# Optimization experiments

Measured on AMD Instinct MI355X. Metric: run time of the kernel, lower is better.

Reference implementation:

```python
import jax, jax.numpy as jnp
import numpy as np

GRID = 48          # static voxel-grid extent (positions generated in [0, GRID)^3)
K = 3              # kernel size per axis (odd -> offset = 0.0 in the original module)
C = (K - 1) // 2   # kernel center
VOXEL_SIZE = 1.0   # forward default in DeConvolution.call


def setup_inputs() -> dict:
    key = jax.random.key(0)
    k1, k2 = jax.random.split(key)
    g = np.arange(GRID)
    coords = np.stack(np.meshgrid(g, g, g, indexing='ij'), axis=-1).reshape(-1, 3)
    # sparse input point cloud: half-density sub-lattice; dense-ish output lattice
    inp_positions = jnp.asarray(coords[coords.sum(axis=1) % 2 == 0], jnp.float32)  # (55296, 3)
    out_positions = jnp.asarray(coords, jnp.float32)                               # (110592, 3)
    n_in = inp_positions.shape[0]
    cin, cout = 256, 256
    features = jax.random.normal(k1, (n_in, cin), dtype=jnp.float32)
    # SparseConvTranspose kernel: [k, k, k, in_channels, filters]
    W = jax.random.normal(k2, (K, K, K, cin, cout), dtype=jnp.float32) * 0.05
    return {"features": features, "inp_positions": inp_positions,
            "out_positions": out_positions, "W": W}


def reference(features, inp_positions, out_positions, W):
    # Voxelize. kernel is odd -> offset = 0.0, so v = floor(p / voxel_size).
    vin = jnp.floor(inp_positions / VOXEL_SIZE).astype(jnp.int32)   # (N_in, 3)
    vout = jnp.floor(out_positions / VOXEL_SIZE).astype(jnp.int32)  # (N_out, 3)
    n_in = features.shape[0]

    # Dense voxel -> input-row hash grid (-1 = empty voxel).
    grid = jnp.full((GRID, GRID, GRID), -1, dtype=jnp.int32)
    grid = grid.at[vin[:, 0], vin[:, 1], vin[:, 2]].set(
        jnp.arange(n_in, dtype=jnp.int32))

    out = jnp.zeros((vout.shape[0], W.shape[-1]), dtype=features.dtype)
    # Transposed sparse conv: out[j] += W[v_in - v_out + C] @ feat[i]
    # Static 27-tap loop; each tap is a gather + dense GEMM.
    for dx in range(-C, C + 1):
        for dy in range(-C, C + 1):
            for dz in range(-C, C + 1):
                u = vout + jnp.array([dx, dy, dz], dtype=jnp.int32)   # source voxel
                inb = jnp.all((u >= 0) & (u < GRID), axis=1)
                uc = jnp.clip(u, 0, GRID - 1)
                idx = grid[uc[:, 0], uc[:, 1], uc[:, 2]]              # (N_out,)
                valid = inb & (idx >= 0)
                g = jnp.where(valid[:, None],
                              features[jnp.maximum(idx, 0)], 0.0)     # (N_out, Cin)
                out = out + g @ W[dx + C, dy + C, dz + C]             # (N_out, Cout)
    return out
```

## Files before the change

kernel.cpp:

```cpp
#include <hip/hip_runtime.h>

#define NIN   55296
#define CIN   256
#define COUT  256
#define NTH   512
#define NBLK  432

typedef __attribute__((ext_vector_type(8))) _Float16 half8;
typedef __attribute__((ext_vector_type(4))) _Float16 half4;
typedef __attribute__((ext_vector_type(4))) float f32x4;

typedef const __attribute__((address_space(1))) void* gp_t;
typedef __attribute__((address_space(3))) void* lp_t;
__device__ __forceinline__ void gload16(const void* g, char* l) {
  __builtin_amdgcn_global_load_lds((gp_t)g, (lp_t)l, 16, 0, 0);
}

__global__ void k_feat_cvt(const float* __restrict__ f, _Float16* __restrict__ o, int n4) {
  int i = blockIdx.x * blockDim.x + threadIdx.x;
  if (i >= n4) return;
  f32x4 v = ((const f32x4*)f)[i];
  half4 r;
  r[0] = (_Float16)v[0]; r[1] = (_Float16)v[1];
  r[2] = (_Float16)v[2]; r[3] = (_Float16)v[3];
  ((half4*)o)[i] = r;
}

__global__ void k_w_cvt(const float* __restrict__ W, _Float16* __restrict__ Wt,
                        float* __restrict__ zeros) {
  int i = blockIdx.x * blockDim.x + threadIdx.x;
  int d   = i >> 16;
  int rem = i & 65535;
  int n   = rem >> 8;
  int k   = rem & 255;
  Wt[i] = (_Float16)W[(d << 16) + (k << 8) + n];
  if (blockIdx.x == 0 && threadIdx.x < 128) zeros[threadIdx.x] = 0.0f;
}

__global__ __launch_bounds__(NTH, 2)
void k_conv8(const _Float16* __restrict__ featb, const _Float16* __restrict__ wt,
             const char* __restrict__ zeros, float* __restrict__ out) {
  extern __shared__ char lds[];
  int* orow = (int*)(lds + 131072);

  const int braw = blockIdx.x;
  const int b    = (braw & 7) * 54 + (braw >> 3);
  const int p    = b & 1;
  const int tile = b >> 1;

  const int tid = threadIdx.x;
  const int w   = tid >> 6;
  const int l   = tid & 63;

  const int rr  = w * 16 + (l >> 2);
  const int swz = ((l & 3) ^ ((l >> 3) & 3)) * 16;

  int xs[2], ys[2], zs[2];
#pragma unroll
  for (int q = 0; q < 2; ++q) {
    int e = tile * 256 + q * 128 + rr;
    int c = e / 24;
    int zi = e - c * 24;
    int x = c / 48;
    int y = c - x * 48;
    xs[q] = x; ys[q] = y; zs[q] = 2 * zi + ((x + y + p) & 1);
  }
  const char* wtc   = (const char*)wt;
  const char* featc = (const char*)featb;
  const int bro0 = rr * 512 + swz;
  const int bro1 = (128 + rr) * 512 + swz;

  const int wm = w >> 2, wn = w & 3;
  const int lr = l & 15, kg = l >> 4;
  const int rsw = (kg ^ ((lr >> 1) & 3)) * 16;
  const int aRd = (wm * 128 + lr) * 64 + rsw;
  const int bRd = (wn * 64 + lr) * 64 + rsw;

  if (tid < 256) {
    int e = tile * 256 + tid;
    int c = e / 24;
    int zi = e - c * 24;
    int x = c / 48;
    int y = c - x * 48;
    int z = 2 * zi + ((x + y + p) & 1);
    orow[tid] = (x * 48 + y) * 48 + z;
  }

  const char* asrc[2];
  const char* wtile;
  auto setoff = [&](int d27) {
    int dx = d27 / 9 - 1, dy = (d27 / 3) % 3 - 1, dz = d27 % 3 - 1;
#pragma unroll
    for (int q = 0; q < 2; ++q) {
      int ux = xs[q] + dx, uy = ys[q] + dy, uz = zs[q] + dz;
      bool v = (unsigned)ux < 48u && (unsigned)uy < 48u && (unsigned)uz < 48u;
      int idx = (ux * 48 + uy) * 24 + (uz >> 1);
      asrc[q] = (v ? (featc + idx * 512) : zeros) + swz;
    }
    wtile = wtc + d27 * 131072;
  };

  int pn = p ? 0 : 1;
  setoff(pn);

  gload16(asrc[0],            lds + 0     + w * 1024);
  gload16(asrc[1],            lds + 8192  + w * 1024);
  gload16(asrc[0] + 64,       lds + 16384 + w * 1024);
  gload16(asrc[1] + 64,       lds + 24576 + w * 1024);
  gload16(wtile + bro0,       lds + 32768 + w * 1024);
  gload16(wtile + bro1,       lds + 40960 + w * 1024);
  gload16(wtile + bro0 + 64,  lds + 49152 + w * 1024);
  gload16(wtile + bro1 + 64,  lds + 57344 + w * 1024);

  f32x4 acc[8][4];
#pragma unroll
  for (int i = 0; i < 8; ++i)
#pragma unroll
    for (int j = 0; j < 4; ++j) acc[i][j] = (f32x4)0.0f;

  const int S = p ? 56 : 52;

  for (int s = 0; s < S; ++s) {
    __syncthreads();

    const char* Ab = lds + (s & 1) * 65536;
    const char* Bb = Ab + 32768;

    const int sn = s + 1;
    if (sn < S) {
      if ((sn & 3) == 0) { pn += 2; setoff(pn); }
      char* Nb = lds + (sn & 1) * 65536;
      const int kb = (sn & 3) * 128;
      gload16(asrc[0] + kb,            Nb + 0     + w * 1024);
      gload16(asrc[1] + kb,            Nb + 8192  + w * 1024);
      gload16(asrc[0] + kb + 64,       Nb + 16384 + w * 1024);
      gload16(asrc[1] + kb + 64,       Nb + 24576 + w * 1024);
      gload16(wtile + bro0 + kb,       Nb + 32768 + w * 1024);
      gload16(wtile + bro1 + kb,       Nb + 40960 + w * 1024);
      gload16(wtile + bro0 + kb + 64,  Nb + 49152 + w * 1024);
      gload16(wtile + bro1 + kb + 64,  Nb + 57344 + w * 1024);
    }

    half8 a[8], b0[4], b1[4];

    b0[0] = *(const half8*)(Bb + bRd);
    b0[1] = *(const half8*)(Bb + bRd + 1024);
#pragma unroll
    for (int mf = 0; mf < 8; ++mf) a[mf] = *(const half8*)(Ab + aRd + mf * 1024);
    b0[2] = *(const half8*)(Bb + bRd + 2048);
    b0[3] = *(const half8*)(Bb + bRd + 3072);
    __builtin_amdgcn_sched_barrier(0);

    __builtin_amdgcn_s_setprio(1);
#pragma unroll
    for (int mf = 0; mf < 8; ++mf) {
      acc[mf][0] = __builtin_amdgcn_mfma_f32_16x16x32_f16(a[mf], b0[0], acc[mf][0], 0, 0, 0);
      acc[mf][1] = __builtin_amdgcn_mfma_f32_16x16x32_f16(a[mf], b0[1], acc[mf][1], 0, 0, 0);
    }
    __builtin_amdgcn_s_setprio(0);

    b1[0] = *(const half8*)(Bb + 16384 + bRd);
    b1[1] = *(const half8*)(Bb + 16384 + bRd + 1024);
    b1[2] = *(const half8*)(Bb + 16384 + bRd + 2048);
    b1[3] = *(const half8*)(Bb + 16384 + bRd + 3072);
    __builtin_amdgcn_sched_barrier(0);

    __builtin_amdgcn_s_setprio(1);
#pragma unroll
    for (int mf = 0; mf < 8; ++mf) {
      acc[mf][2] = __builtin_amdgcn_mfma_f32_16x16x32_f16(a[mf], b0[2], acc[mf][2], 0, 0, 0);
      acc[mf][3] = __builtin_amdgcn_mfma_f32_16x16x32_f16(a[mf], b0[3], acc[mf][3], 0, 0, 0);
      a[mf] = *(const half8*)(Ab + 16384 + aRd + mf * 1024);
    }
    __builtin_amdgcn_s_setprio(0);
    __builtin_amdgcn_sched_barrier(0);

    __builtin_amdgcn_s_setprio(1);
#pragma unroll
    for (int mf = 0; mf < 8; ++mf) {
      acc[mf][0] = __builtin_amdgcn_mfma_f32_16x16x32_f16(a[mf], b1[0], acc[mf][0], 0, 0, 0);
      acc[mf][1] = __builtin_amdgcn_mfma_f32_16x16x32_f16(a[mf], b1[1], acc[mf][1], 0, 0, 0);
    }
    __builtin_amdgcn_s_setprio(0);
    __builtin_amdgcn_sched_barrier(0);

    __builtin_amdgcn_s_setprio(1);
#pragma unroll
    for (int mf = 0; mf < 8; ++mf) {
      acc[mf][2] = __builtin_amdgcn_mfma_f32_16x16x32_f16(a[mf], b1[2], acc[mf][2], 0, 0, 0);
      acc[mf][3] = __builtin_amdgcn_mfma_f32_16x16x32_f16(a[mf], b1[3], acc[mf][3], 0, 0, 0);
    }
    __builtin_amdgcn_s_setprio(0);
  }

#pragma unroll
  for (int mf = 0; mf < 8; ++mf) {
#pragma unroll
    for (int i = 0; i < 4; ++i) {
      int r = wm * 128 + mf * 16 + kg * 4 + i;
      int o = orow[r];
      float* dst = out + (size_t)o * COUT + wn * 64 + lr;
#pragma unroll
      for (int nf = 0; nf < 4; ++nf) dst[nf * 16] = acc[mf][nf][i];
    }
  }
}

extern "C" void kernel_launch(void* const* d_in, const int* in_sizes, int n_in,
                              void* d_out, int out_size, void* d_ws, size_t ws_size,
                              hipStream_t stream) {
  const float* features = (const float*)d_in[0];
  const float* W = (const float*)d_in[3];
  float* out = (float*)d_out;

  char* ws = (char*)d_ws;
  _Float16* featb = (_Float16*)ws;
  _Float16* Wt    = (_Float16*)(ws + 28311552);
  float*    zeros = (float*)(ws + 28311552 + 3538944);

  (void)hipFuncSetAttribute(reinterpret_cast<const void*>(k_conv8),
                            hipFuncAttributeMaxDynamicSharedMemorySize, 132096);

  {
    int n4 = NIN * CIN / 4;
    k_feat_cvt<<<(n4 + 255) / 256, 256, 0, stream>>>(features, featb, n4);
  }
  k_w_cvt<<<27 * 65536 / 256, 256, 0, stream>>>(W, Wt, zeros);

  k_conv8<<<NBLK, NTH, 132096, stream>>>(featb, Wt, (const char*)zeros, out);
}
```

Before: 208.1 us.

## Load weight fragments directly from global into registers instead of via LDS

Weight (B) tiles are no longer staged through LDS with async global-to-LDS copies. Each wave now reads its B fragments straight from global or L2 into registers at the start of every k-step. This halves the LDS footprint, which could allow more blocks per CU, and removes the LDS reads for B. The cost is global load latency sitting directly on the critical path before the MFMAs, with no prefetch, and redundant weight reads across the two waves that share the same B columns.

Measured after the change: 340.2 us. +63.5%, slower.

```diff
diff --git a/kernel.cpp b/kernel.cpp
--- a/kernel.cpp
+++ b/kernel.cpp
@@ -41,7 +41,7 @@
 void k_conv8(const _Float16* __restrict__ featb, const _Float16* __restrict__ wt,
              const char* __restrict__ zeros, float* __restrict__ out) {
   extern __shared__ char lds[];
-  int* orow = (int*)(lds + 131072);
+  int* orow = (int*)(lds + 65536);
 
   const int braw = blockIdx.x;
   const int b    = (braw & 7) * 54 + (braw >> 3);
@@ -67,14 +67,12 @@
   }
   const char* wtc   = (const char*)wt;
   const char* featc = (const char*)featb;
-  const int bro0 = rr * 512 + swz;
-  const int bro1 = (128 + rr) * 512 + swz;
 
   const int wm = w >> 2, wn = w & 3;
   const int lr = l & 15, kg = l >> 4;
   const int rsw = (kg ^ ((lr >> 1) & 3)) * 16;
   const int aRd = (wm * 128 + lr) * 64 + rsw;
-  const int bRd = (wn * 64 + lr) * 64 + rsw;
+  const int bq  = (wn * 64 + lr) * 512 + kg * 16;
 
   if (tid < 256) {
     int e = tile * 256 + tid;
@@ -87,7 +85,6 @@
   }
 
   const char* asrc[2];
-  const char* wtile;
   auto setoff = [&](int d27) {
     int dx = d27 / 9 - 1, dy = (d27 / 3) % 3 - 1, dz = d27 % 3 - 1;
 #pragma unroll
@@ -97,20 +94,16 @@
       int idx = (ux * 48 + uy) * 24 + (uz >> 1);
       asrc[q] = (v ? (featc + idx * 512) : zeros) + swz;
     }
-    wtile = wtc + d27 * 131072;
   };
 
-  int pn = p ? 0 : 1;
+  const int pb = p ? 0 : 1;
+  int pn = pb;
   setoff(pn);
 
-  gload16(asrc[0],            lds + 0     + w * 1024);
-  gload16(asrc[1],            lds + 8192  + w * 1024);
-  gload16(asrc[0] + 64,       lds + 16384 + w * 1024);
-  gload16(asrc[1] + 64,       lds + 24576 + w * 1024);
-  gload16(wtile + bro0,       lds + 32768 + w * 1024);
-  gload16(wtile + bro1,       lds + 40960 + w * 1024);
-  gload16(wtile + bro0 + 64,  lds + 49152 + w * 1024);
-  gload16(wtile + bro1 + 64,  lds + 57344 + w * 1024);
+  gload16(asrc[0],      lds + 0     + w * 1024);
+  gload16(asrc[1],      lds + 8192  + w * 1024);
+  gload16(asrc[0] + 64, lds + 16384 + w * 1024);
+  gload16(asrc[1] + 64, lds + 24576 + w * 1024);
 
   f32x4 acc[8][4];
 #pragma unroll
@@ -123,53 +116,51 @@
   for (int s = 0; s < S; ++s) {
     __syncthreads();
 
-    const char* Ab = lds + (s & 1) * 65536;
-    const char* Bb = Ab + 32768;
+    const char* Ab = lds + (s & 1) * 32768;
+
+    const char* wk = wtc + (pb + ((s >> 2) << 1)) * 131072 + (s & 3) * 128 + bq;
+    half8 bf[8];
+    bf[0] = *(const half8*)(wk);
+    bf[1] = *(const half8*)(wk + 8192);
+    bf[2] = *(const half8*)(wk + 16384);
+    bf[3] = *(const half8*)(wk + 24576);
+    bf[4] = *(const half8*)(wk + 64);
+    bf[5] = *(const half8*)(wk + 8256);
+    bf[6] = *(const half8*)(wk + 16448);
+    bf[7] = *(const half8*)(wk + 24640);
+    __builtin_amdgcn_sched_barrier(0);
 
     const int sn = s + 1;
     if (sn < S) {
       if ((sn & 3) == 0) { pn += 2; setoff(pn); }
-      char* Nb = lds + (sn & 1) * 65536;
+      char* Nb = lds + (sn & 1) * 32768;
       const int kb = (sn & 3) * 128;
-      gload16(asrc[0] + kb,            Nb + 0     + w * 1024);
-      gload16(asrc[1] + kb,            Nb + 8192  + w * 1024);
-      gload16(asrc[0] + kb + 64,       Nb + 16384 + w * 1024);
-      gload16(asrc[1] + kb + 64,       Nb + 24576 + w * 1024);
-      gload16(wtile + bro0 + kb,       Nb + 32768 + w * 1024);
-      gload16(wtile + bro1 + kb,       Nb + 40960 + w * 1024);
-      gload16(wtile + bro0 + kb + 64,  Nb + 49152 + w * 1024);
-      gload16(wtile + bro1 + kb + 64,  Nb + 57344 + w * 1024);
-    }
-
-    half8 a[8], b0[4], b1[4];
-
-    b0[0] = *(const half8*)(Bb + bRd);
-    b0[1] = *(const half8*)(Bb + bRd + 1024);
+      gload16(asrc[0] + kb,      Nb + 0     + w * 1024);
+      gload16(asrc[1] + kb,      Nb + 8192  + w * 1024);
+      gload16(asrc[0] + kb + 64, Nb + 16384 + w * 1024);
+      gload16(asrc[1] + kb + 64, Nb + 24576 + w * 1024);
+    }
+    __builtin_amdgcn_sched_barrier(0);
+
+    half8 a[8];
 #pragma unroll
     for (int mf = 0; mf < 8; ++mf) a[mf] = *(const half8*)(Ab + aRd + mf * 1024);
-    b0[2] = *(const half8*)(Bb + bRd + 2048);
-    b0[3] = *(const half8*)(Bb + bRd + 3072);
-    __builtin_amdgcn_sched_barrier(0);
-
-    __builtin_amdgcn_s_setprio(1);
-#pragma unroll
-    for (int mf = 0; mf < 8; ++mf) {
-      acc[mf][0] = __builtin_amdgcn_mfma_f32_16x16x32_f16(a[mf], b0[0], acc[mf][0], 0, 0, 0);
-      acc[mf][1] = __builtin_amdgcn_mfma_f32_16x16x32_f16(a[mf], b0[1], acc[mf][1], 0, 0, 0);
-    }
-    __builtin_amdgcn_s_setprio(0);
-
-    b1[0] = *(const half8*)(Bb + 16384 + bRd);
-    b1[1] = *(const half8*)(Bb + 16384 + bRd + 1024);
-    b1[2] = *(const half8*)(Bb + 16384 + bRd + 2048);
-    b1[3] = *(const half8*)(Bb + 16384 + bRd + 3072);
-    __builtin_amdgcn_sched_barrier(0);
-
-    __builtin_amdgcn_s_setprio(1);
-#pragma unroll
-    for (int mf = 0; mf < 8; ++mf) {
-      acc[mf][2] = __builtin_amdgcn_mfma_f32_16x16x32_f16(a[mf], b0[2], acc[mf][2], 0, 0, 0);
-      acc[mf][3] = __builtin_amdgcn_mfma_f32_16x16x32_f16(a[mf], b0[3], acc[mf][3], 0, 0, 0);
+    __builtin_amdgcn_sched_barrier(0);
+
+    __builtin_amdgcn_s_setprio(1);
+#pragma unroll
+    for (int mf = 0; mf < 8; ++mf) {
+      acc[mf][0] = __builtin_amdgcn_mfma_f32_16x16x32_f16(a[mf], bf[0], acc[mf][0], 0, 0, 0);
+      acc[mf][1] = __builtin_amdgcn_mfma_f32_16x16x32_f16(a[mf], bf[1], acc[mf][1], 0, 0, 0);
+    }
+    __builtin_amdgcn_s_setprio(0);
+    __builtin_amdgcn_sched_barrier(0);
+
+    __builtin_amdgcn_s_setprio(1);
+#pragma unroll
+    for (int mf = 0; mf < 8; ++mf) {
+      acc[mf][2] = __builtin_amdgcn_mfma_f32_16x16x32_f16(a[mf], bf[2], acc[mf][2], 0, 0, 0);
+      acc[mf][3] = __builtin_amdgcn_mfma_f32_16x16x32_f16(a[mf], bf[3], acc[mf][3], 0, 0, 0);
       a[mf] = *(const half8*)(Ab + 16384 + aRd + mf * 1024);
     }
     __builtin_amdgcn_s_setprio(0);
@@ -178,17 +169,17 @@
     __builtin_amdgcn_s_setprio(1);
 #pragma unroll
     for (int mf = 0; mf < 8; ++mf) {
-      acc[mf][0] = __builtin_amdgcn_mfma_f32_16x16x32_f16(a[mf], b1[0], acc[mf][0], 0, 0, 0);
-      acc[mf][1] = __builtin_amdgcn_mfma_f32_16x16x32_f16(a[mf], b1[1], acc[mf][1], 0, 0, 0);
-    }
-    __builtin_amdgcn_s_setprio(0);
-    __builtin_amdgcn_sched_barrier(0);
-
-    __builtin_amdgcn_s_setprio(1);
-#pragma unroll
-    for (int mf = 0; mf < 8; ++mf) {
-      acc[mf][2] = __builtin_amdgcn_mfma_f32_16x16x32_f16(a[mf], b1[2], acc[mf][2], 0, 0, 0);
-      acc[mf][3] = __builtin_amdgcn_mfma_f32_16x16x32_f16(a[mf], b1[3], acc[mf][3], 0, 0, 0);
+      acc[mf][0] = __builtin_amdgcn_mfma_f32_16x16x32_f16(a[mf], bf[4], acc[mf][0], 0, 0, 0);
+      acc[mf][1] = __builtin_amdgcn_mfma_f32_16x16x32_f16(a[mf], bf[5], acc[mf][1], 0, 0, 0);
+    }
+    __builtin_amdgcn_s_setprio(0);
+    __builtin_amdgcn_sched_barrier(0);
+
+    __builtin_amdgcn_s_setprio(1);
+#pragma unroll
+    for (int mf = 0; mf < 8; ++mf) {
+      acc[mf][2] = __builtin_amdgcn_mfma_f32_16x16x32_f16(a[mf], bf[6], acc[mf][2], 0, 0, 0);
+      acc[mf][3] = __builtin_amdgcn_mfma_f32_16x16x32_f16(a[mf], bf[7], acc[mf][3], 0, 0, 0);
     }
     __builtin_amdgcn_s_setprio(0);
   }
@@ -219,7 +210,7 @@
   float*    zeros = (float*)(ws + 28311552 + 3538944);
 
   (void)hipFuncSetAttribute(reinterpret_cast<const void*>(k_conv8),
-                            hipFuncAttributeMaxDynamicSharedMemorySize, 132096);
+                            hipFuncAttributeMaxDynamicSharedMemorySize, 66560);
 
   {
     int n4 = NIN * CIN / 4;
@@ -227,5 +218,5 @@
   }
   k_w_cvt<<<27 * 65536 / 256, 256, 0, stream>>>(W, Wt, zeros);
 
-  k_conv8<<<NBLK, NTH, 132096, stream>>>(featb, Wt, (const char*)zeros, out);
-}
+  k_conv8<<<NBLK, NTH, 66560, stream>>>(featb, Wt, (const char*)zeros, out);
+}
```
